# Kernel tuning notes

Measured on AMD Instinct MI355X. Metric: run time of the kernel, lower is better.

## Reference

```python
import jax, jax.numpy as jnp
import numpy as np

B, L, D, H, NL, FUT, MD = 4096, 64, 16, 128, 2, 30, 2
HEAD_IN = D + H  # 144


def setup_inputs() -> dict:
    key = jax.random.key(0)
    ks = jax.random.split(key, 20)
    g = lambda k, *sh: jax.random.normal(k, sh, dtype=jnp.float32) * 0.05
    return {
        'history': jax.random.normal(ks[0], (B, L, D), dtype=jnp.float32),
        'history_mask': jnp.ones((B, L), dtype=jnp.float32),
        'Wp': g(ks[1], D, H), 'bp': jnp.zeros((H,), jnp.float32),
        # stacked gate weights: order [f, i, o, c]
        'Wx': g(ks[2], NL, 4, H, H), 'bx': jnp.zeros((NL, 4, H), jnp.float32),
        'Uh': g(ks[3], NL, 4, H, H),
        'Wd': g(ks[4], NL, H, H), 'bd': jnp.zeros((NL, H), jnp.float32),
        'Wt': g(ks[5], NL, H), 'bt': jnp.zeros((NL, H), jnp.float32),
        'ln_g': jnp.ones((HEAD_IN,), jnp.float32), 'ln_b': jnp.zeros((HEAD_IN,), jnp.float32),
        'W1': g(ks[6], HEAD_IN, H), 'b1': jnp.zeros((H,), jnp.float32),
        'W2': g(ks[7], H, FUT * MD), 'b2': jnp.zeros((FUT * MD,), jnp.float32),
    }


def _forward(history, history_mask, Wp, bp, Wx, bx, Uh, Wd, bd, Wt, bt,
             ln_g, ln_b, W1, b1, W2, b2):
    x = history @ Wp + bp                                 # [B,L,H]
    delta = jnp.clip(history[..., 5], 0.0)[..., None]     # [B,L,1]
    mask = history_mask[..., None]                        # [B,L,1]
    e = jnp.float32(np.e)

    def step(carry, inp):
        h, c = carry                                      # each [NL,B,H]
        xt, dt, mt = inp                                  # [B,H],[B,1],[B,1]
        decay = 1.0 / jnp.log(e + dt)                     # [B,1]
        step_in = xt
        hs, cs = [], []
        for l in range(NL):
            z = (jnp.einsum('bh,ghk->gbk', step_in, Wx[l]) + bx[l][:, None, :]
                 + jnp.einsum('bh,ghk->gbk', h[l], Uh[l]))  # [4,B,H]
            f_t = jax.nn.sigmoid(z[0])
            i_t = jax.nn.sigmoid(z[1])
            o_t = jax.nn.sigmoid(z[2])
            c_tilde = jnp.tanh(z[3])
            h_tilde = c_tilde + i_t
            h_short = jnp.tanh(h_tilde @ Wd[l] + bd[l])
            d_t = jax.nn.sigmoid(decay * Wt[l] + bt[l])   # [B,H]
            h_star = (h_tilde - h_short) + h_short * d_t
            c_new = jnp.tanh(h_star + o_t * c[l])
            h_new = o_t * jnp.tanh(c_new)
            h_l = mt * h_new + (1.0 - mt) * h[l]
            c_l = mt * c_new + (1.0 - mt) * c[l]
            hs.append(h_l)
            cs.append(c_l)
            step_in = h_l
        return (jnp.stack(hs), jnp.stack(cs)), step_in

    h0 = jnp.zeros((NL, B, H), x.dtype)
    c0 = jnp.zeros((NL, B, H), x.dtype)
    xs = (x.transpose(1, 0, 2), delta.transpose(1, 0, 2), mask.transpose(1, 0, 2))
    _, outs = jax.lax.scan(step, (h0, c0), xs)            # [L,B,H]
    encoded = outs.transpose(1, 0, 2) * mask              # [B,L,H]

    # decoder state: last valid obs + hidden
    counts = jnp.clip(history_mask.sum(axis=1), 1, L).astype(jnp.int32)
    last = counts - 1
    bi = jnp.arange(B)
    state = jnp.concatenate([history[bi, last, :], encoded[bi, last, :]], axis=-1)

    # forecast head: LayerNorm -> Linear -> ReLU -> Linear
    mu = state.mean(axis=-1, keepdims=True)
    var = state.var(axis=-1, keepdims=True)
    sn = (state - mu) * jax.lax.rsqrt(var + 1e-5) * ln_g + ln_b
    pred = jax.nn.relu(sn @ W1 + b1) @ W2 + b2
    pred = pred.reshape(B, FUT, MD)
    return jnp.nan_to_num(pred, nan=0.0, posinf=1e4, neginf=-1e4)


def reference(history, history_mask, Wp, bp, Wx, bx, Uh, Wd, bd, Wt, bt,
              ln_g, ln_b, W1, b1, W2, b2):
    return _forward(history, history_mask, Wp, bp, Wx, bx, Uh, Wd, bd, Wt, bt,
                    ln_g, ln_b, W1, b1, W2, b2)
```

## Files before the change

kernel.cpp:

```cpp
#include <hip/hip_runtime.h>
#include <hip/hip_bf16.h>


typedef __bf16 bf16x8 __attribute__((ext_vector_type(8)));
typedef float  f32x4  __attribute__((ext_vector_type(4)));

__device__ __forceinline__ f32x4 mfma16(bf16x8 a, bf16x8 b, f32x4 c) {
  return __builtin_amdgcn_mfma_f32_16x16x32_bf16(a, b, c, 0, 0, 0);
}

#if __has_builtin(__builtin_amdgcn_exp2f)
__device__ __forceinline__ float fexp2(float x) { return __builtin_amdgcn_exp2f(x); }
#else
__device__ __forceinline__ float fexp2(float x) { return exp2f(x); }
#endif
#if __has_builtin(__builtin_amdgcn_rcpf)
__device__ __forceinline__ float frcp(float x) { return __builtin_amdgcn_rcpf(x); }
#else
__device__ __forceinline__ float frcp(float x) { return __fdividef(1.f, x); }
#endif
__device__ __forceinline__ float sigmf(float x) {
  return frcp(1.f + fexp2(-1.44269504f * x));
}
__device__ __forceinline__ float tanhfast(float x) {
  return __fmaf_rn(-2.f, frcp(1.f + fexp2(2.88539008f * x)), 1.f);
}

#define OFF_BWD0 129024
#define OFF_BT1  161792
#define OFF_BWD1 358400
#define OFF_BZ0  391168

#define S_WB0   0
#define S_AH    129024
#define S_A0H   131584
#define S_A1H   135936
#define S_AT0   140288
#define S_AT1   144640
#define S_DM    148992
#define S_LAST  149248
#define S_TOTAL 149312
#define S_STATE 0
#define S_A1L   9216
#define S_REDS  17408
#define S_REDQ  18432

__global__ void tlstm_fold(const float* __restrict__ Wp, const float* __restrict__ bp,
                           const float* __restrict__ Wx, const float* __restrict__ bx,
                           __bf16* __restrict__ BT0, float* __restrict__ bz0) {
  int idx = blockIdx.x * 256 + threadIdx.x;
  if (idx >= 384 * 17) return;
  int n = idx / 17, kk = idx % 17;
  int npr = n & 127, gs = (n >> 7) + 1;
  const float* wxcol = Wx + (gs * 128) * 128 + npr;
  if (kk < 16) {
    const float* wprow = Wp + kk * 128;
    float s = 0.f;
    for (int h = 0; h < 128; ++h) s += wprow[h] * wxcol[h * 128];
    BT0[n * 168 + kk] = (__bf16)s;
  } else {
    float s = bx[gs * 128 + npr];
    for (int h = 0; h < 128; ++h) s += bp[h] * wxcol[h * 128];
    bz0[n] = s;
    for (int k2 = 16; k2 < 32; ++k2) BT0[n * 168 + k2] = (__bf16)0.f;
  }
}

__global__ void tlstm_pack(const float* __restrict__ Wx, const float* __restrict__ Uh,
                           const float* __restrict__ Wd,
                           __bf16* __restrict__ BT0, __bf16* __restrict__ BWd0,
                           __bf16* __restrict__ BT1, __bf16* __restrict__ BWd1) {
  int e = blockIdx.x * 256 + threadIdx.x;
  if (e < 49152) {
    int n = e >> 7, k = e & 127, npr = n & 127, gs = (n >> 7) + 1;
    BT0[n * 168 + 32 + k] = (__bf16)Uh[(gs * 128 + k) * 128 + npr];
  } else if (e < 65536) {
    int e2 = e - 49152; int n = e2 >> 7, k = e2 & 127;
    BWd0[n * 128 + k] = (__bf16)Wd[k * 128 + n];
  } else if (e < 163840) {
    int e2 = e - 65536; int n = e2 >> 8, k = e2 & 255;
    int npr = n & 127, gs = (n >> 7) + 1;
    float v = (k < 128) ? Wx[((4 + gs) * 128 + k) * 128 + npr]
                        : Uh[((4 + gs) * 128 + (k - 128)) * 128 + npr];
    BT1[n * 256 + k] = (__bf16)v;
  } else if (e < 180224) {
    int e2 = e - 163840; int n = e2 >> 7, k = e2 & 127;
    BWd1[n * 128 + k] = (__bf16)Wd[(128 + k) * 128 + n];
  }
}

__global__ __launch_bounds__(512, 1) void tlstm_main(
    const float* __restrict__ hist, const float* __restrict__ hmask,
    const __bf16* __restrict__ BT0, const __bf16* __restrict__ BWd0,
    const __bf16* __restrict__ BT1, const __bf16* __restrict__ BWd1,
    const float* __restrict__ bz0, const float* __restrict__ bx,
    const float* __restrict__ bd, const float* __restrict__ Wt,
    const float* __restrict__ bt, const float* __restrict__ lng,
    const float* __restrict__ lnb, const float* __restrict__ W1,
    const float* __restrict__ b1, const float* __restrict__ W2,
    const float* __restrict__ b2, float* __restrict__ out) {
  extern __shared__ __align__(16) char smem[];
  __bf16* WB0 = (__bf16*)(smem + S_WB0);
  __bf16 (*AH)[16][40]  = (__bf16(*)[16][40])(smem + S_AH);
  __bf16 (*A0H)[136]    = (__bf16(*)[136])(smem + S_A0H);
  __bf16 (*A1H)[136]    = (__bf16(*)[136])(smem + S_A1H);
  __bf16 (*AT0)[136]    = (__bf16(*)[136])(smem + S_AT0);
  __bf16 (*AT1)[136]    = (__bf16(*)[136])(smem + S_AT1);
  float (*dmL)[2][16]   = (float(*)[2][16])(smem + S_DM);
  int*   lastL          = (int*)(smem + S_LAST);
  float (*stateL)[144]  = (float(*)[144])(smem + S_STATE);
  float (*a1L)[128]     = (float(*)[128])(smem + S_A1L);
  float (*redS)[16]     = (float(*)[16])(smem + S_REDS);
  float (*redQ)[16]     = (float(*)[16])(smem + S_REDQ);

  const int tid  = threadIdx.x;
  const int wave = tid >> 6;
  const int lane = tid & 63;
  const int q    = lane >> 4;
  const int c16  = lane & 15;
  const int q8   = q * 8;
  const int b0   = blockIdx.x * 16;
  const int nc   = wave * 16 + c16;

  for (int i = tid * 8; i < 64512; i += 4096)
    *(bf16x8*)(WB0 + i) = *(const bf16x8*)(BT0 + i);
  {
    __bf16* z = (__bf16*)(smem + S_AH);
    for (int i = tid; i < 5632; i += 512) z[i] = (__bf16)0.f;
  }
  if (tid < 16) {
    float s = 0.f;
    for (int t = 0; t < 64; ++t) s += hmask[(b0 + tid) * 64 + t];
    s = fminf(fmaxf(s, 1.f), 64.f);
    lastL[tid] = (int)s - 1;
  }

  float bz0r[3], bz1r[3];
#pragma unroll
  for (int g = 0; g < 3; ++g) {
    bz0r[g] = bz0[g * 128 + nc];
    bz1r[g] = bx[(5 + g) * 128 + nc];
  }
  const float bd0r = bd[nc],      bd1r = bd[128 + nc];
  const float wt0r = Wt[nc],      wt1r = Wt[128 + nc];
  const float bt0r = bt[nc],      bt1r = bt[128 + nc];

  int offZ0[3];
#pragma unroll
  for (int g = 0; g < 3; ++g) offZ0[g] = (g * 128 + nc) * 168;

  bf16x8 wf1[24], bwd0[4], bwd1[4];
#pragma unroll
  for (int g = 0; g < 3; ++g)
#pragma unroll
    for (int kk = 0; kk < 8; ++kk)
      wf1[g * 8 + kk] = *(const bf16x8*)(BT1 + (g * 128 + nc) * 256 + kk * 32 + q8);
#pragma unroll
  for (int kk = 0; kk < 4; ++kk) {
    bwd0[kk] = *(const bf16x8*)(BWd0 + nc * 128 + q8 + kk * 32);
    bwd1[kk] = *(const bf16x8*)(BWd1 + nc * 128 + q8 + kk * 32);
  }

  float h0r[4] = {}, c0r[4] = {}, h1r[4] = {}, c1r[4] = {}, encr[4] = {};

  __syncthreads();

  int lrow[4];
#pragma unroll
  for (int r = 0; r < 4; ++r) lrow[r] = lastL[q * 4 + r];

  const int srow = (tid >> 4) & 15, scol = tid & 15;
  const float* histrow = hist + (long)(b0 + srow) * 1024 + scol;
  const float* hmrow   = hmask + (long)(b0 + srow) * 64;

  float hv = 0.f, mv = 0.f;
  if (tid < 256) {
    float v0 = histrow[0];
    AH[0][srow][scol] = (__bf16)v0;
    if (scol == 5)
      dmL[0][0][srow] = __fdividef(1.f, __logf(2.7182818284590452f + fmaxf(v0, 0.f)));
    if (scol == 0) dmL[0][1][srow] = hmrow[0];
    hv = histrow[16];
    mv = hmrow[1];
  }
  __syncthreads();

  for (int t = 0; t <= 64; ++t) {
    const int p = t & 1, pn = p ^ 1;

    float dpre[4], mpre[4];
    if (t > 0) {
#pragma unroll
      for (int r = 0; r < 4; ++r) {
        dpre[r] = dmL[pn][0][q * 4 + r];
        mpre[r] = dmL[pn][1][q * 4 + r];
      }
    }

    float htl0[4], otl0[4], htl1[4], otl1[4];
    if (t > 0) {
      f32x4 acc[3];
#pragma unroll
      for (int g = 0; g < 3; ++g) acc[g] = (f32x4){bz1r[g], bz1r[g], bz1r[g], bz1r[g]};
#pragma unroll
      for (int kk = 0; kk < 4; ++kk) {
        bf16x8 a = *(const bf16x8*)&A0H[c16][kk * 32 + q8];
#pragma unroll
        for (int g = 0; g < 3; ++g) acc[g] = mfma16(a, wf1[g * 8 + kk], acc[g]);
      }
#pragma unroll
      for (int kk = 4; kk < 8; ++kk) {
        bf16x8 a = *(const bf16x8*)&A1H[c16][(kk - 4) * 32 + q8];
#pragma unroll
        for (int g = 0; g < 3; ++g) acc[g] = mfma16(a, wf1[g * 8 + kk], acc[g]);
      }
#pragma unroll
      for (int r = 0; r < 4; ++r) {
        float ht = tanhfast(acc[2][r]) + sigmf(acc[0][r]);
        htl1[r] = ht;
        otl1[r] = sigmf(acc[1][r]);
        AT1[q * 4 + r][nc] = (__bf16)ht;
      }
    }
    if (t < 64) {
      f32x4 acc[3];
#pragma unroll
      for (int g = 0; g < 3; ++g) acc[g] = (f32x4){bz0r[g], bz0r[g], bz0r[g], bz0r[g]};
      {
        bf16x8 a = *(const bf16x8*)&AH[p][c16][q8];
#pragma unroll
        for (int g = 0; g < 3; ++g)
          acc[g] = mfma16(a, *(const bf16x8*)(WB0 + offZ0[g] + q8), acc[g]);
      }
#pragma unroll
      for (int kk = 0; kk < 4; ++kk) {
        bf16x8 a = *(const bf16x8*)&A0H[c16][kk * 32 + q8];
#pragma unroll
        for (int g = 0; g < 3; ++g)
          acc[g] = mfma16(a, *(const bf16x8*)(WB0 + offZ0[g] + 32 + kk * 32 + q8), acc[g]);
      }
#pragma unroll
      for (int r = 0; r < 4; ++r) {
        float ht = tanhfast(acc[2][r]) + sigmf(acc[0][r]);
        htl0[r] = ht;
        otl0[r] = sigmf(acc[1][r]);
        AT0[q * 4 + r][nc] = (__bf16)ht;
      }
    }
    __syncthreads();

    if (t < 64) {
      float drow[4], mrow[4];
#pragma unroll
      for (int r = 0; r < 4; ++r) {
        drow[r] = dmL[p][0][q * 4 + r];
        mrow[r] = dmL[p][1][q * 4 + r];
      }
      f32x4 accd = (f32x4){bd0r, bd0r, bd0r, bd0r};
#pragma unroll
      for (int kk = 0; kk < 4; ++kk) {
        bf16x8 a = *(const bf16x8*)&AT0[c16][kk * 32 + q8];
        accd = mfma16(a, bwd0[kk], accd);
      }
#pragma unroll
      for (int r = 0; r < 4; ++r) {
        float hs    = tanhfast(accd[r]);
        float dgate = sigmf(__fmaf_rn(drow[r], wt0r, bt0r));
        float hstar = __fmaf_rn(hs, dgate - 1.f, htl0[r]);
        float cn    = tanhfast(__fmaf_rn(otl0[r], c0r[r], hstar));
        float hn    = otl0[r] * tanhfast(cn);
        float m     = mrow[r];
        float hl    = __fmaf_rn(m, hn - h0r[r], h0r[r]);
        float cl    = __fmaf_rn(m, cn - c0r[r], c0r[r]);
        h0r[r] = hl; c0r[r] = cl;
        A0H[q * 4 + r][nc] = (__bf16)hl;
      }
    }
    if (t > 0) {
      f32x4 accd = (f32x4){bd1r, bd1r, bd1r, bd1r};
#pragma unroll
      for (int kk = 0; kk < 4; ++kk) {
        bf16x8 a = *(const bf16x8*)&AT1[c16][kk * 32 + q8];
        accd = mfma16(a, bwd1[kk], accd);
      }
      const int tm1 = t - 1;
#pragma unroll
      for (int r = 0; r < 4; ++r) {
        float hs    = tanhfast(accd[r]);
        float dgate = sigmf(__fmaf_rn(dpre[r], wt1r, bt1r));
        float hstar = __fmaf_rn(hs, dgate - 1.f, htl1[r]);
        float cn    = tanhfast(__fmaf_rn(otl1[r], c1r[r], hstar));
        float hn    = otl1[r] * tanhfast(cn);
        float m     = mpre[r];
        float hl    = __fmaf_rn(m, hn - h1r[r], h1r[r]);
        float cl    = __fmaf_rn(m, cn - c1r[r], c1r[r]);
        h1r[r] = hl; c1r[r] = cl;
        A1H[q * 4 + r][nc] = (__bf16)hl;
        if (tm1 == lrow[r]) encr[r] = hl * m;
      }
    }
    if (tid < 256 && t < 63) {
      AH[pn][srow][scol] = (__bf16)hv;
      if (scol == 5)
        dmL[pn][0][srow] = __fdividef(1.f, __logf(2.7182818284590452f + fmaxf(hv, 0.f)));
      if (scol == 0) dmL[pn][1][srow] = mv;
      if (t < 62) { hv = histrow[(t + 2) * 16]; mv = hmrow[t + 2]; }
    }
    __syncthreads();
  }

  if (tid < 256)
    stateL[srow][scol] = hist[((long)(b0 + srow) * 64 + lastL[srow]) * 16 + scol];
#pragma unroll
  for (int r = 0; r < 4; ++r)
    stateL[q * 4 + r][16 + nc] = encr[r];
  __syncthreads();

  if (tid < 256) {
    float sm = 0.f, sq = 0.f;
    for (int k = scol; k < 144; k += 16) {
      float v = stateL[srow][k];
      sm += v; sq += v * v;
    }
    redS[srow][scol] = sm; redQ[srow][scol] = sq;
  }
  __syncthreads();
  if (tid < 16) {
    float sm = 0.f, sq = 0.f;
    for (int s2 = 0; s2 < 16; ++s2) { sm += redS[tid][s2]; sq += redQ[tid][s2]; }
    float mu  = sm * (1.f / 144.f);
    float var = sq * (1.f / 144.f) - mu * mu;
    redS[0][tid] = mu;
    redQ[0][tid] = rsqrtf(var + 1e-5f);
  }
  __syncthreads();
  if (tid < 256) {
    float mu = redS[0][srow], rs = redQ[0][srow];
    for (int k = scol; k < 144; k += 16)
      stateL[srow][k] = (stateL[srow][k] - mu) * rs * lng[k] + lnb[k];
  }
  __syncthreads();
  if (tid < 256) {
    float accw[8];
#pragma unroll
    for (int o = 0; o < 8; ++o) accw[o] = b1[scol + 16 * o];
    for (int k = 0; k < 144; ++k) {
      float sv = stateL[srow][k];
      const float* w = W1 + k * 128 + scol;
#pragma unroll
      for (int o = 0; o < 8; ++o) accw[o] += sv * w[16 * o];
    }
#pragma unroll
    for (int o = 0; o < 8; ++o) a1L[srow][scol + 16 * o] = fmaxf(accw[o], 0.f);
  }
  __syncthreads();
  for (int e = tid; e < 960; e += 512) {
    int row = e / 60, j = e - row * 60;
    float accv = b2[j];
    for (int k = 0; k < 128; ++k) accv += a1L[row][k] * W2[k * 60 + j];
    accv = (accv != accv) ? 0.f : fminf(fmaxf(accv, -1e4f), 1e4f);
    out[(b0 + row) * 60 + j] = accv;
  }
}

extern "C" void kernel_launch(void* const* d_in, const int* in_sizes, int n_in,
                              void* d_out, int out_size, void* d_ws, size_t ws_size,
                              hipStream_t stream) {
  const float* hist  = (const float*)d_in[0];
  const float* hmask = (const float*)d_in[1];
  const float* Wp    = (const float*)d_in[2];
  const float* bp    = (const float*)d_in[3];
  const float* Wx    = (const float*)d_in[4];
  const float* bx    = (const float*)d_in[5];
  const float* Uh    = (const float*)d_in[6];
  const float* Wd    = (const float*)d_in[7];
  const float* bd    = (const float*)d_in[8];
  const float* Wt    = (const float*)d_in[9];
  const float* bt    = (const float*)d_in[10];
  const float* lng   = (const float*)d_in[11];
  const float* lnb   = (const float*)d_in[12];
  const float* W1    = (const float*)d_in[13];
  const float* b1    = (const float*)d_in[14];
  const float* W2    = (const float*)d_in[15];
  const float* b2    = (const float*)d_in[16];
  float* out = (float*)d_out;

  char* ws = (char*)d_ws;
  __bf16* BT0  = (__bf16*)ws;
  __bf16* BWd0 = (__bf16*)(ws + OFF_BWD0);
  __bf16* BT1  = (__bf16*)(ws + OFF_BT1);
  __bf16* BWd1 = (__bf16*)(ws + OFF_BWD1);
  float*  bz0  = (float*)(ws + OFF_BZ0);

  hipFuncSetAttribute((const void*)tlstm_main,
                      hipFuncAttributeMaxDynamicSharedMemorySize, S_TOTAL);

  tlstm_fold<<<26, 256, 0, stream>>>(Wp, bp, Wx, bx, BT0, bz0);
  tlstm_pack<<<704, 256, 0, stream>>>(Wx, Uh, Wd, BT0, BWd0, BT1, BWd1);
  tlstm_main<<<256, 512, S_TOTAL, stream>>>(hist, hmask, BT0, BWd0, BT1, BWd1,
                                            bz0, bx, bd, Wt, bt, lng, lnb,
                                            W1, b1, W2, b2, out);
}
```

Before: 316.3 us.

## Prescale gate weights into exp2 domain and swizzle layer-0 LDS weights

Folds the exp2 scaling constants for sigmoid and tanh into the packed gate weights, biases and decay parameters at pack time, which drops a multiply per activation in the recurrent loop. The layer-0 weight tile in LDS is reordered into an MFMA fragment-friendly layout without padding, so each lane reads contiguous 16-byte chunks and shared memory use shrinks. The A-operand fragments are loaded once per step and shared by both layers, and the decay/mask buffer becomes triple-buffered. Scaling before bf16 rounding changes numerics slightly, and the extra register pressure from hoisted fragments is a risk.

```diff
diff --git a/kernel.cpp b/kernel.cpp
--- a/kernel.cpp
+++ b/kernel.cpp
@@ -19,79 +19,88 @@
 #else
 __device__ __forceinline__ float frcp(float x) { return __fdividef(1.f, x); }
 #endif
-__device__ __forceinline__ float sigmf(float x) {
-  return frcp(1.f + fexp2(-1.44269504f * x));
-}
-__device__ __forceinline__ float tanhfast(float x) {
-  return __fmaf_rn(-2.f, frcp(1.f + fexp2(2.88539008f * x)), 1.f);
-}
-
-#define OFF_BWD0 129024
-#define OFF_BT1  161792
-#define OFF_BWD1 358400
-#define OFF_BZ0  391168
+__device__ __forceinline__ float sigmE(float u) { return frcp(1.f + fexp2(u)); }
+__device__ __forceinline__ float tanhE(float u) {
+  return __fmaf_rn(-2.f, frcp(1.f + fexp2(u)), 1.f);
+}
+#define SCL_S (-1.44269504f)
+#define SCL_T (2.88539008f)
+
+#define OFF_BWD0 122880
+#define OFF_BT1  155648
+#define OFF_BWD1 352256
+#define OFF_BZ0  385024
 
 #define S_WB0   0
-#define S_AH    129024
-#define S_A0H   131584
-#define S_A1H   135936
-#define S_AT0   140288
-#define S_AT1   144640
-#define S_DM    148992
-#define S_LAST  149248
-#define S_TOTAL 149312
+#define S_AH    122880
+#define S_A0H   125440
+#define S_A1H   129792
+#define S_AT0   134144
+#define S_AT1   138496
+#define S_DM    142848
+#define S_LAST  143232
+#define S_TOTAL 143296
 #define S_STATE 0
 #define S_A1L   9216
 #define S_REDS  17408
 #define S_REDQ  18432
 
+__device__ __forceinline__ int bt0f_off(int n, int k) {
+  int g = n >> 7, w = (n >> 4) & 7, c = n & 15;
+  int kk = k >> 5, q = (k >> 3) & 3, j = k & 7;
+  return ((w * 3 + g) * 5 + kk) * 512 + (q * 16 + c) * 8 + j;
+}
+
 __global__ void tlstm_fold(const float* __restrict__ Wp, const float* __restrict__ bp,
                            const float* __restrict__ Wx, const float* __restrict__ bx,
-                           __bf16* __restrict__ BT0, float* __restrict__ bz0) {
+                           __bf16* __restrict__ BT0f, float* __restrict__ bz0) {
   int idx = blockIdx.x * 256 + threadIdx.x;
   if (idx >= 384 * 17) return;
   int n = idx / 17, kk = idx % 17;
-  int npr = n & 127, gs = (n >> 7) + 1;
+  int npr = n & 127, g = n >> 7, gs = g + 1;
+  float sg = (g == 2) ? SCL_T : SCL_S;
   const float* wxcol = Wx + (gs * 128) * 128 + npr;
   if (kk < 16) {
     const float* wprow = Wp + kk * 128;
     float s = 0.f;
     for (int h = 0; h < 128; ++h) s += wprow[h] * wxcol[h * 128];
-    BT0[n * 168 + kk] = (__bf16)s;
+    BT0f[bt0f_off(n, kk)] = (__bf16)(s * sg);
   } else {
     float s = bx[gs * 128 + npr];
     for (int h = 0; h < 128; ++h) s += bp[h] * wxcol[h * 128];
-    bz0[n] = s;
-    for (int k2 = 16; k2 < 32; ++k2) BT0[n * 168 + k2] = (__bf16)0.f;
+    bz0[n] = s * sg;
+    for (int k2 = 16; k2 < 32; ++k2) BT0f[bt0f_off(n, k2)] = (__bf16)0.f;
   }
 }
 
 __global__ void tlstm_pack(const float* __restrict__ Wx, const float* __restrict__ Uh,
                            const float* __restrict__ Wd,
-                           __bf16* __restrict__ BT0, __bf16* __restrict__ BWd0,
+                           __bf16* __restrict__ BT0f, __bf16* __restrict__ BWd0,
                            __bf16* __restrict__ BT1, __bf16* __restrict__ BWd1) {
   int e = blockIdx.x * 256 + threadIdx.x;
   if (e < 49152) {
-    int n = e >> 7, k = e & 127, npr = n & 127, gs = (n >> 7) + 1;
-    BT0[n * 168 + 32 + k] = (__bf16)Uh[(gs * 128 + k) * 128 + npr];
+    int n = e >> 7, k = e & 127, npr = n & 127, g = n >> 7, gs = g + 1;
+    float sg = (g == 2) ? SCL_T : SCL_S;
+    BT0f[bt0f_off(n, k + 32)] = (__bf16)(Uh[(gs * 128 + k) * 128 + npr] * sg);
   } else if (e < 65536) {
     int e2 = e - 49152; int n = e2 >> 7, k = e2 & 127;
-    BWd0[n * 128 + k] = (__bf16)Wd[k * 128 + n];
+    BWd0[n * 128 + k] = (__bf16)(Wd[k * 128 + n] * SCL_T);
   } else if (e < 163840) {
     int e2 = e - 65536; int n = e2 >> 8, k = e2 & 255;
-    int npr = n & 127, gs = (n >> 7) + 1;
+    int npr = n & 127, g = n >> 7, gs = g + 1;
+    float sg = (g == 2) ? SCL_T : SCL_S;
     float v = (k < 128) ? Wx[((4 + gs) * 128 + k) * 128 + npr]
                         : Uh[((4 + gs) * 128 + (k - 128)) * 128 + npr];
-    BT1[n * 256 + k] = (__bf16)v;
+    BT1[n * 256 + k] = (__bf16)(v * sg);
   } else if (e < 180224) {
     int e2 = e - 163840; int n = e2 >> 7, k = e2 & 127;
-    BWd1[n * 128 + k] = (__bf16)Wd[(128 + k) * 128 + n];
+    BWd1[n * 128 + k] = (__bf16)(Wd[(128 + k) * 128 + n] * SCL_T);
   }
 }
 
 __global__ __launch_bounds__(512, 1) void tlstm_main(
     const float* __restrict__ hist, const float* __restrict__ hmask,
-    const __bf16* __restrict__ BT0, const __bf16* __restrict__ BWd0,
+    const __bf16* __restrict__ BT0f, const __bf16* __restrict__ BWd0,
     const __bf16* __restrict__ BT1, const __bf16* __restrict__ BWd1,
     const float* __restrict__ bz0, const float* __restrict__ bx,
     const float* __restrict__ bd, const float* __restrict__ Wt,
@@ -122,8 +131,8 @@
   const int b0   = blockIdx.x * 16;
   const int nc   = wave * 16 + c16;
 
-  for (int i = tid * 8; i < 64512; i += 4096)
-    *(bf16x8*)(WB0 + i) = *(const bf16x8*)(BT0 + i);
+  for (int i = tid * 8; i < 61440; i += 4096)
+    *(bf16x8*)(WB0 + i) = *(const bf16x8*)(BT0f + i);
   {
     __bf16* z = (__bf16*)(smem + S_AH);
     for (int i = tid; i < 5632; i += 512) z[i] = (__bf16)0.f;
@@ -138,16 +147,17 @@
   float bz0r[3], bz1r[3];
 #pragma unroll
   for (int g = 0; g < 3; ++g) {
+    float sg = (g == 2) ? SCL_T : SCL_S;
     bz0r[g] = bz0[g * 128 + nc];
-    bz1r[g] = bx[(5 + g) * 128 + nc];
-  }
-  const float bd0r = bd[nc],      bd1r = bd[128 + nc];
-  const float wt0r = Wt[nc],      wt1r = Wt[128 + nc];
-  const float bt0r = bt[nc],      bt1r = bt[128 + nc];
-
-  int offZ0[3];
-#pragma unroll
-  for (int g = 0; g < 3; ++g) offZ0[g] = (g * 128 + nc) * 168;
+    bz1r[g] = bx[(5 + g) * 128 + nc] * sg;
+  }
+  const float bd0r = bd[nc] * SCL_T,       bd1r = bd[128 + nc] * SCL_T;
+  const float wt0r = Wt[nc] * SCL_S,       wt1r = Wt[128 + nc] * SCL_S;
+  const float bt0r = bt[nc] * SCL_S,       bt1r = bt[128 + nc] * SCL_S;
+
+  int offW[3];
+#pragma unroll
+  for (int g = 0; g < 3; ++g) offW[g] = ((wave * 3 + g) * 5) * 512 + lane * 8;
 
   bf16x8 wf1[24], bwd0[4], bwd1[4];
 #pragma unroll
@@ -187,15 +197,15 @@
 
   for (int t = 0; t <= 64; ++t) {
     const int p = t & 1, pn = p ^ 1;
-
-    float dpre[4], mpre[4];
-    if (t > 0) {
-#pragma unroll
-      for (int r = 0; r < 4; ++r) {
-        dpre[r] = dmL[pn][0][q * 4 + r];
-        mpre[r] = dmL[pn][1][q * 4 + r];
-      }
-    }
+    const int sp = t % 3, sm = (t + 2) % 3, sn = (t + 1) % 3;
+
+    bf16x8 a0h[4], a1h[4], ahf;
+#pragma unroll
+    for (int kk = 0; kk < 4; ++kk) {
+      a0h[kk] = *(const bf16x8*)&A0H[c16][kk * 32 + q8];
+      a1h[kk] = *(const bf16x8*)&A1H[c16][kk * 32 + q8];
+    }
+    ahf = *(const bf16x8*)&AH[p][c16][q8];
 
     float htl0[4], otl0[4], htl1[4], otl1[4];
     if (t > 0) {
@@ -203,22 +213,18 @@
 #pragma unroll
       for (int g = 0; g < 3; ++g) acc[g] = (f32x4){bz1r[g], bz1r[g], bz1r[g], bz1r[g]};
 #pragma unroll
-      for (int kk = 0; kk < 4; ++kk) {
-        bf16x8 a = *(const bf16x8*)&A0H[c16][kk * 32 + q8];
-#pragma unroll
-        for (int g = 0; g < 3; ++g) acc[g] = mfma16(a, wf1[g * 8 + kk], acc[g]);
-      }
-#pragma unroll
-      for (int kk = 4; kk < 8; ++kk) {
-        bf16x8 a = *(const bf16x8*)&A1H[c16][(kk - 4) * 32 + q8];
-#pragma unroll
-        for (int g = 0; g < 3; ++g) acc[g] = mfma16(a, wf1[g * 8 + kk], acc[g]);
-      }
-#pragma unroll
-      for (int r = 0; r < 4; ++r) {
-        float ht = tanhfast(acc[2][r]) + sigmf(acc[0][r]);
+      for (int kk = 0; kk < 4; ++kk)
+#pragma unroll
+        for (int g = 0; g < 3; ++g) acc[g] = mfma16(a0h[kk], wf1[g * 8 + kk], acc[g]);
+#pragma unroll
+      for (int kk = 0; kk < 4; ++kk)
+#pragma unroll
+        for (int g = 0; g < 3; ++g) acc[g] = mfma16(a1h[kk], wf1[g * 8 + 4 + kk], acc[g]);
+#pragma unroll
+      for (int r = 0; r < 4; ++r) {
+        float ht = tanhE(acc[2][r]) + sigmE(acc[0][r]);
         htl1[r] = ht;
-        otl1[r] = sigmf(acc[1][r]);
+        otl1[r] = sigmE(acc[1][r]);
         AT1[q * 4 + r][nc] = (__bf16)ht;
       }
     }
@@ -226,24 +232,19 @@
       f32x4 acc[3];
 #pragma unroll
       for (int g = 0; g < 3; ++g) acc[g] = (f32x4){bz0r[g], bz0r[g], bz0r[g], bz0r[g]};
-      {
-        bf16x8 a = *(const bf16x8*)&AH[p][c16][q8];
+#pragma unroll
+      for (int g = 0; g < 3; ++g)
+        acc[g] = mfma16(ahf, *(const bf16x8*)(WB0 + offW[g]), acc[g]);
+#pragma unroll
+      for (int kk = 0; kk < 4; ++kk)
 #pragma unroll
         for (int g = 0; g < 3; ++g)
-          acc[g] = mfma16(a, *(const bf16x8*)(WB0 + offZ0[g] + q8), acc[g]);
-      }
-#pragma unroll
-      for (int kk = 0; kk < 4; ++kk) {
-        bf16x8 a = *(const bf16x8*)&A0H[c16][kk * 32 + q8];
-#pragma unroll
-        for (int g = 0; g < 3; ++g)
-          acc[g] = mfma16(a, *(const bf16x8*)(WB0 + offZ0[g] + 32 + kk * 32 + q8), acc[g]);
-      }
-#pragma unroll
-      for (int r = 0; r < 4; ++r) {
-        float ht = tanhfast(acc[2][r]) + sigmf(acc[0][r]);
+          acc[g] = mfma16(a0h[kk], *(const bf16x8*)(WB0 + offW[g] + (kk + 1) * 512), acc[g]);
+#pragma unroll
+      for (int r = 0; r < 4; ++r) {
+        float ht = tanhE(acc[2][r]) + sigmE(acc[0][r]);
         htl0[r] = ht;
-        otl0[r] = sigmf(acc[1][r]);
+        otl0[r] = sigmE(acc[1][r]);
         AT0[q * 4 + r][nc] = (__bf16)ht;
       }
     }
@@ -253,8 +254,8 @@
       float drow[4], mrow[4];
 #pragma unroll
       for (int r = 0; r < 4; ++r) {
-        drow[r] = dmL[p][0][q * 4 + r];
-        mrow[r] = dmL[p][1][q * 4 + r];
+        drow[r] = dmL[sp][0][q * 4 + r];
+        mrow[r] = dmL[sp][1][q * 4 + r];
       }
       f32x4 accd = (f32x4){bd0r, bd0r, bd0r, bd0r};
 #pragma unroll
@@ -264,11 +265,11 @@
       }
 #pragma unroll
       for (int r = 0; r < 4; ++r) {
-        float hs    = tanhfast(accd[r]);
-        float dgate = sigmf(__fmaf_rn(drow[r], wt0r, bt0r));
+        float hs    = tanhE(accd[r]);
+        float dgate = sigmE(__fmaf_rn(drow[r], wt0r, bt0r));
         float hstar = __fmaf_rn(hs, dgate - 1.f, htl0[r]);
-        float cn    = tanhfast(__fmaf_rn(otl0[r], c0r[r], hstar));
-        float hn    = otl0[r] * tanhfast(cn);
+        float cn    = tanhE(SCL_T * __fmaf_rn(otl0[r], c0r[r], hstar));
+        float hn    = otl0[r] * tanhE(SCL_T * cn);
         float m     = mrow[r];
         float hl    = __fmaf_rn(m, hn - h0r[r], h0r[r]);
         float cl    = __fmaf_rn(m, cn - c0r[r], c0r[r]);
@@ -277,6 +278,12 @@
       }
     }
     if (t > 0) {
+      float dpre[4], mpre[4];
+#pragma unroll
+      for (int r = 0; r < 4; ++r) {
+        dpre[r] = dmL[sm][0][q * 4 + r];
+        mpre[r] = dmL[sm][1][q * 4 + r];
+      }
       f32x4 accd = (f32x4){bd1r, bd1r, bd1r, bd1r};
 #pragma unroll
       for (int kk = 0; kk < 4; ++kk) {
@@ -286,11 +293,11 @@
       const int tm1 = t - 1;
 #pragma unroll
       for (int r = 0; r < 4; ++r) {
-        float hs    = tanhfast(accd[r]);
-        float dgate = sigmf(__fmaf_rn(dpre[r], wt1r, bt1r));
+        float hs    = tanhE(accd[r]);
+        float dgate = sigmE(__fmaf_rn(dpre[r], wt1r, bt1r));
         float hstar = __fmaf_rn(hs, dgate - 1.f, htl1[r]);
-        float cn    = tanhfast(__fmaf_rn(otl1[r], c1r[r], hstar));
-        float hn    = otl1[r] * tanhfast(cn);
+        float cn    = tanhE(SCL_T * __fmaf_rn(otl1[r], c1r[r], hstar));
+        float hn    = otl1[r] * tanhE(SCL_T * cn);
         float m     = mpre[r];
         float hl    = __fmaf_rn(m, hn - h1r[r], h1r[r]);
         float cl    = __fmaf_rn(m, cn - c1r[r], c1r[r]);
@@ -302,8 +309,8 @@
     if (tid < 256 && t < 63) {
       AH[pn][srow][scol] = (__bf16)hv;
       if (scol == 5)
-        dmL[pn][0][srow] = __fdividef(1.f, __logf(2.7182818284590452f + fmaxf(hv, 0.f)));
-      if (scol == 0) dmL[pn][1][srow] = mv;
+        dmL[sn][0][srow] = __fdividef(1.f, __logf(2.7182818284590452f + fmaxf(hv, 0.f)));
+      if (scol == 0) dmL[sn][1][srow] = mv;
       if (t < 62) { hv = histrow[(t + 2) * 16]; mv = hmrow[t + 2]; }
     }
     __syncthreads();
@@ -317,18 +324,18 @@
   __syncthreads();
 
   if (tid < 256) {
-    float sm = 0.f, sq = 0.f;
+    float sm2 = 0.f, sq = 0.f;
     for (int k = scol; k < 144; k += 16) {
       float v = stateL[srow][k];
-      sm += v; sq += v * v;
-    }
-    redS[srow][scol] = sm; redQ[srow][scol] = sq;
+      sm2 += v; sq += v * v;
+    }
+    redS[srow][scol] = sm2; redQ[srow][scol] = sq;
   }
   __syncthreads();
   if (tid < 16) {
-    float sm = 0.f, sq = 0.f;
-    for (int s2 = 0; s2 < 16; ++s2) { sm += redS[tid][s2]; sq += redQ[tid][s2]; }
-    float mu  = sm * (1.f / 144.f);
+    float sm2 = 0.f, sq = 0.f;
+    for (int s2 = 0; s2 < 16; ++s2) { sm2 += redS[tid][s2]; sq += redQ[tid][s2]; }
+    float mu  = sm2 * (1.f / 144.f);
     float var = sq * (1.f / 144.f) - mu * mu;
     redS[0][tid] = mu;
     redQ[0][tid] = rsqrtf(var + 1e-5f);
@@ -386,7 +393,7 @@
   float* out = (float*)d_out;
 
   char* ws = (char*)d_ws;
-  __bf16* BT0  = (__bf16*)ws;
+  __bf16* BT0f = (__bf16*)ws;
   __bf16* BWd0 = (__bf16*)(ws + OFF_BWD0);
   __bf16* BT1  = (__bf16*)(ws + OFF_BT1);
   __bf16* BWd1 = (__bf16*)(ws + OFF_BWD1);
@@ -395,9 +402,9 @@
   hipFuncSetAttribute((const void*)tlstm_main,
                       hipFuncAttributeMaxDynamicSharedMemorySize, S_TOTAL);
 
-  tlstm_fold<<<26, 256, 0, stream>>>(Wp, bp, Wx, bx, BT0, bz0);
-  tlstm_pack<<<704, 256, 0, stream>>>(Wx, Uh, Wd, BT0, BWd0, BT1, BWd1);
-  tlstm_main<<<256, 512, S_TOTAL, stream>>>(hist, hmask, BT0, BWd0, BT1, BWd1,
+  tlstm_fold<<<26, 256, 0, stream>>>(Wp, bp, Wx, bx, BT0f, bz0);
+  tlstm_pack<<<704, 256, 0, stream>>>(Wx, Uh, Wd, BT0f, BWd0, BT1, BWd1);
+  tlstm_main<<<256, 512, S_TOTAL, stream>>>(hist, hmask, BT0f, BWd0, BT1, BWd1,
                                             bz0, bx, bd, Wt, bt, lng, lnb,
                                             W1, b1, W2, b2, out);
 }
```

Result: no change. 310.7 us (-1.8%).
